# Kernel tuning notes

Measured on AMD Instinct MI355X. Metric: run time of the kernel, lower is better.

## Reference

```python
import jax, jax.numpy as jnp
import numpy as np

# Production-scale dims: ViT patch attention on a 32x32 patch grid
B, L, F = 16, 1024, 512      # batch, seq (=NX*NY patches), model dim
H, D = 8, 64                 # heads, head_dim (F = H*D)
NX, NY = 32, 32              # patch grid; Toeplitz table size 4*NX*NY = 4096


def setup_inputs() -> dict:
    key = jax.random.key(0)
    ks = jax.random.split(key, 12)
    w = lambda k, shp: jax.random.normal(k, shp, jnp.float32) * 0.02
    return {
        "inputs_q": jax.random.normal(ks[0], (B, L, F), jnp.float32),
        "inputs_kv": jax.random.normal(ks[1], (B, L, F), jnp.float32),
        "Wq": w(ks[2], (F, H * D)), "bq": jnp.zeros((H * D,), jnp.float32),
        "Wk": w(ks[3], (F, H * D)), "bk": jnp.zeros((H * D,), jnp.float32),
        "Wv": w(ks[4], (F, H * D)), "bv": jnp.zeros((H * D,), jnp.float32),
        "Wo": w(ks[5], (H * D, F)), "bo": jnp.zeros((F,), jnp.float32),
        "toeplitz": w(ks[6], (H, 4 * NX * NY)),
    }


def _rel_index():
    # 2D relative-position (Toeplitz) index: patch p -> (x, y) on NX x NY grid.
    coords = jnp.arange(L)
    xi, yi = coords // NY, coords % NY
    dx = xi[:, None] - xi[None, :] + NX          # in [1, 2*NX-1]
    dy = yi[:, None] - yi[None, :] + NY          # in [1, 2*NY-1]
    return dx * (2 * NY) + dy                    # [L, L] indices into 4*NX*NY table


def reference(inputs_q, inputs_kv, Wq, bq, Wk, bk, Wv, bv, Wo, bo, toeplitz):
    q = (inputs_q @ Wq + bq).reshape(B, L, H, D)
    k = (inputs_kv @ Wk + bk).reshape(B, L, H, D)
    v = (inputs_kv @ Wv + bv).reshape(B, L, H, D)
    bias = toeplitz[:, _rel_index()]             # [H, L, L] Toeplitz relative bias
    scale = 1.0 / jnp.sqrt(jnp.float32(D))
    scores = jnp.einsum("bqhd,bkhd->bhqk", q, k) * scale + bias  # [B,H,L,L]
    attn = jax.nn.softmax(scores, axis=-1)
    x = jnp.einsum("bhqk,bkhd->bqhd", attn, v).reshape(B, L, H * D)
    out = x @ Wo + bo
    return out.reshape(B, L, H, D)               # matches torch forward's final reshape
```

## Files before the change

### kernel.cpp

```cpp
#include <hip/hip_runtime.h>
#include <hip/hip_bf16.h>

#define B_  16
#define L_  1024
#define F_  512
#define H_  8
#define D_  64
#define M_  (B_ * L_)
#define HD_ 512

typedef __bf16 bf16x8 __attribute__((ext_vector_type(8)));
typedef __bf16 bf16x4 __attribute__((ext_vector_type(4)));
typedef short  s16x4  __attribute__((ext_vector_type(4)));
typedef float  f32x4  __attribute__((ext_vector_type(4)));

__device__ __forceinline__ void gl_lds16(const void* g, void* l) {
  __builtin_amdgcn_global_load_lds(
      (const __attribute__((address_space(1))) unsigned int*)g,
      (__attribute__((address_space(3))) unsigned int*)l, 16, 0, 0);
}

__global__ __launch_bounds__(256) void wt_kernel(
    const float* __restrict__ Wq, const float* __restrict__ Wk,
    const float* __restrict__ Wv, const float* __restrict__ Wo,
    __bf16* __restrict__ Wt_all)
{
  const float* W = (blockIdx.z == 0) ? Wq : (blockIdx.z == 1) ? Wk
                 : (blockIdx.z == 2) ? Wv : Wo;
  __bf16* Wt = Wt_all + (size_t)blockIdx.z * (512 * 512);
  __shared__ float s[32][33];
  const int t = threadIdx.x;
  const int r = t >> 5, c = t & 31;
  const int k0 = blockIdx.x * 32, n0 = blockIdx.y * 32;
#pragma unroll
  for (int i = 0; i < 4; ++i)
    s[r + i * 8][c] = W[(size_t)(k0 + r + i * 8) * 512 + n0 + c];
  __syncthreads();
#pragma unroll
  for (int i = 0; i < 4; ++i)
    Wt[(size_t)(n0 + r + i * 8) * 512 + k0 + c] = (__bf16)s[c][r + i * 8];
}

__global__ __launch_bounds__(256) void cvt_kernel(
    const float* __restrict__ xq, const float* __restrict__ xkv,
    __bf16* __restrict__ oq, __bf16* __restrict__ okv)
{
  const float* src = blockIdx.y ? xkv : xq;
  __bf16* dst = blockIdx.y ? okv : oq;
  size_t i = ((size_t)blockIdx.x * 256 + threadIdx.x) * 8;
  float4 f0 = *(const float4*)(src + i);
  float4 f1 = *(const float4*)(src + i + 4);
  bf16x8 v;
  v[0] = (__bf16)f0.x; v[1] = (__bf16)f0.y; v[2] = (__bf16)f0.z; v[3] = (__bf16)f0.w;
  v[4] = (__bf16)f1.x; v[5] = (__bf16)f1.y; v[6] = (__bf16)f1.z; v[7] = (__bf16)f1.w;
  *(bf16x8*)(dst + i) = v;
}

__global__ __launch_bounds__(256, 4) void gemm_proj_kernel(
    const __bf16* __restrict__ Xq, const __bf16* __restrict__ Xkv,
    const __bf16* __restrict__ Wt_all,
    const float* __restrict__ bq, const float* __restrict__ bk_,
    const float* __restrict__ bv_,
    __bf16* __restrict__ qd, __bf16* __restrict__ kd, __bf16* __restrict__ vd)
{
  const int seg = blockIdx.y >> 2;
  const __bf16* X = (seg == 0) ? Xq : Xkv;
  const __bf16* Wt = Wt_all + (size_t)seg * 262144;
  const float* bias = (seg == 0) ? bq : (seg == 1) ? bk_ : bv_;
  __bf16* dst = (seg == 0) ? qd : (seg == 1) ? kd : vd;
  const int mode = seg;

  __shared__ __align__(16) __bf16 As[2][4][128][8];
  __shared__ __align__(16) __bf16 Bs[2][4][128][8];
  const int t = threadIdx.x;
  const int m0 = blockIdx.x * 128, n0 = (blockIdx.y & 3) * 128;
  const int lane = t & 63, w = t >> 6;
  const int ml = lane & 15, quad = lane >> 4;
  const int wm = w & 1, wn = w >> 1;

  f32x4 acc[4][4];
#pragma unroll
  for (int i = 0; i < 4; ++i)
#pragma unroll
    for (int j = 0; j < 4; ++j) acc[i][j] = (f32x4){0.f, 0.f, 0.f, 0.f};

  const int slot0 = w * 64 + lane;
  const int slot1 = (w + 4) * 64 + lane;
  const int ko0 = slot0 >> 7, row0_ = slot0 & 127;
  const int ko1 = slot1 >> 7, row1_ = slot1 & 127;

#define STAGE_PROJ(buf, kk)                                                     \
  do {                                                                          \
    gl_lds16(&X[(size_t)(m0 + row0_) * 512 + (kk) + ko0 * 8],                   \
             &As[buf][ko0][row0_][0]);                                          \
    gl_lds16(&Wt[(size_t)(n0 + row0_) * 512 + (kk) + ko0 * 8],                  \
             &Bs[buf][ko0][row0_][0]);                                          \
    gl_lds16(&X[(size_t)(m0 + row1_) * 512 + (kk) + ko1 * 8],                   \
             &As[buf][ko1][row1_][0]);                                          \
    gl_lds16(&Wt[(size_t)(n0 + row1_) * 512 + (kk) + ko1 * 8],                  \
             &Bs[buf][ko1][row1_][0]);                                          \
  } while (0)

#define COMPUTE_TILE(buf)                                                       \
  do {                                                                          \
    bf16x8 a[4], b[4];                                                          \
    _Pragma("unroll") for (int mt = 0; mt < 4; ++mt)                            \
        a[mt] = *(const bf16x8*)&As[buf][quad][wm * 64 + mt * 16 + ml][0];      \
    _Pragma("unroll") for (int nt = 0; nt < 4; ++nt)                            \
        b[nt] = *(const bf16x8*)&Bs[buf][quad][wn * 64 + nt * 16 + ml][0];      \
    _Pragma("unroll") for (int mt = 0; mt < 4; ++mt)                            \
        _Pragma("unroll") for (int nt = 0; nt < 4; ++nt)                        \
            acc[mt][nt] = __builtin_amdgcn_mfma_f32_16x16x32_bf16(              \
                a[mt], b[nt], acc[mt][nt], 0, 0, 0);                            \
  } while (0)

  STAGE_PROJ(0, 0);
#pragma unroll
  for (int tt = 0; tt < 15; ++tt) {
    const int cur = tt & 1;
    STAGE_PROJ(cur ^ 1, (tt + 1) * 32);
    asm volatile("s_waitcnt vmcnt(4)" ::: "memory");
    asm volatile("s_barrier" ::: "memory");
    COMPUTE_TILE(cur);
    asm volatile("s_barrier" ::: "memory");
  }
  asm volatile("s_waitcnt vmcnt(0)" ::: "memory");
  asm volatile("s_barrier" ::: "memory");
  COMPUTE_TILE(1);

#pragma unroll
  for (int nt = 0; nt < 4; ++nt) {
    int col = n0 + wn * 64 + nt * 16 + ml;
    float bv = bias[col];
    int h = col >> 6, d = col & 63;
#pragma unroll
    for (int mt = 0; mt < 4; ++mt) {
      int row0 = m0 + wm * 64 + mt * 16 + quad * 4;
      int bz = row0 >> 10;
      int l0 = row0 & 1023;
      if (mode == 2) {
        bf16x4 pk;
#pragma unroll
        for (int r = 0; r < 4; ++r) pk[r] = (__bf16)(acc[mt][nt][r] + bv);
        size_t idx = ((size_t)(bz * H_ + h) * D_ + d) * L_ + l0;
        *(bf16x4*)&dst[idx] = pk;
      } else {
        size_t base = ((size_t)(bz * H_ + h) * L_ + l0) * D_ + d;
#pragma unroll
        for (int r = 0; r < 4; ++r)
          dst[base + (size_t)r * D_] = (__bf16)(acc[mt][nt][r] + bv);
      }
    }
  }
#undef STAGE_PROJ
#undef COMPUTE_TILE
}

__global__ __launch_bounds__(256, 2) void attn_kernel(
    const __bf16* __restrict__ qg,
    const __bf16* __restrict__ kg,
    const __bf16* __restrict__ vg,
    const float* __restrict__ toep_g,
    __bf16* __restrict__ xg)
{
  __shared__ float toep[4096];
  __shared__ __align__(16) __bf16 Ks[2][64][64];
  __shared__ __align__(16) __bf16 Vs[2][64][64];

  const int t = threadIdx.x;
  const int n = blockIdx.x;
  const int bh = ((n >> 5) << 3) | (n & 7);
  const int q0 = ((n >> 3) & 3) * 256;
  const int h = bh & 7;
  const int lane = t & 63, w = t >> 6;
  const int ml = lane & 15, quad = lane >> 4;
  const int lo3 = lane >> 3;
  const int kop = lane & 7;

  const size_t qkbase = (size_t)bh * (L_ * D_);
  const size_t vbase  = (size_t)bh * (D_ * L_);

  {
    const float4* src = (const float4*)(toep_g + (size_t)h * 4096);
    float4* dl = (float4*)toep;
    for (int i = t; i < 1024; i += 256) dl[i] = src[i];
  }

#pragma unroll
  for (int i = 0; i < 2; ++i) {
    int row = (w * 2 + i) * 8 + lo3;
    int ko = kop ^ lo3;
    gl_lds16(&kg[qkbase + (size_t)row * D_ + ko * 8], &Ks[0][row][kop * 8]);
    gl_lds16(&vg[vbase + (size_t)row * L_ + ko * 8], &Vs[0][row][kop * 8]);
  }

  bf16x8 qf[4][2];
#pragma unroll
  for (int qn = 0; qn < 4; ++qn) {
    const __bf16* qp =
        qg + qkbase + (size_t)(q0 + w * 64 + qn * 16 + ml) * D_ + quad * 8;
    qf[qn][0] = *(const bf16x8*)qp;
    qf[qn][1] = *(const bf16x8*)(qp + 32);
  }

  float lpart[4] = {0.f, 0.f, 0.f, 0.f};
  f32x4 o[4][4];
#pragma unroll
  for (int qn = 0; qn < 4; ++qn)
#pragma unroll
    for (int dt = 0; dt < 4; ++dt) o[qn][dt] = (f32x4){0.f, 0.f, 0.f, 0.f};

  __syncthreads();

  int cur = 0;
  for (int k0 = 0; k0 < L_; k0 += 64) {
    if (k0 + 64 < L_) {
      int nb = cur ^ 1;
#pragma unroll
      for (int i = 0; i < 2; ++i) {
        int row = (w * 2 + i) * 8 + lo3;
        int ko = kop ^ lo3;
        gl_lds16(&kg[qkbase + (size_t)(k0 + 64 + row) * D_ + ko * 8],
                 &Ks[nb][row][kop * 8]);
        gl_lds16(&vg[vbase + (size_t)row * L_ + k0 + 64 + ko * 8],
                 &Vs[nb][row][kop * 8]);
      }
    }

#pragma unroll
    for (int nt = 0; nt < 4; ++nt) {
      bf16x8 kf0 = *(const bf16x8*)&Ks[cur][nt * 16 + ml][(quad ^ (ml & 7)) * 8];
      bf16x8 kf1 =
          *(const bf16x8*)&Ks[cur][nt * 16 + ml][((4 + quad) ^ (ml & 7)) * 8];
      int kx = (k0 >> 5) + (nt >> 1);

      s16x4 pfrag[4];
#pragma unroll
      for (int qn = 0; qn < 4; ++qn) {
        f32x4 z = (f32x4){0.f, 0.f, 0.f, 0.f};
        z = __builtin_amdgcn_mfma_f32_16x16x32_bf16(kf0, qf[qn][0], z, 0, 0, 0);
        z = __builtin_amdgcn_mfma_f32_16x16x32_bf16(kf1, qf[qn][1], z, 0, 0, 0);

        int qb = w * 64 + qn * 16;
        int base = (((q0 + qb) >> 5) - kx + 32) * 64 +
                   ((qb & 31) + ml - ((nt & 1) * 16 + quad * 4) + 32);
        float p[4];
#pragma unroll
        for (int r = 0; r < 4; ++r)
          p[r] = __expf(fmaf(z[r], 0.125f, toep[base - r]));
        lpart[qn] += (p[0] + p[1]) + (p[2] + p[3]);
        bf16x4 pk;
#pragma unroll
        for (int r = 0; r < 4; ++r) pk[r] = (__bf16)p[r];
        pfrag[qn] = __builtin_bit_cast(s16x4, pk);
      }

#pragma unroll
      for (int dt = 0; dt < 4; ++dt) {
        int row = dt * 16 + ml;
        int gc = nt * 2 + (quad >> 1);
        bf16x4 vfr = *(const bf16x4*)
            &Vs[cur][row][((gc ^ (row & 7)) * 8) + (quad & 1) * 4];
        s16x4 vfs = __builtin_bit_cast(s16x4, vfr);
#pragma unroll
        for (int qn = 0; qn < 4; ++qn)
          o[qn][dt] = __builtin_amdgcn_mfma_f32_16x16x16bf16_1k(
              pfrag[qn], vfs, o[qn][dt], 0, 0, 0);
      }
    }

    __syncthreads();
    cur ^= 1;
  }

#pragma unroll
  for (int qn = 0; qn < 4; ++qn) {
    lpart[qn] += __shfl_xor(lpart[qn], 16);
    lpart[qn] += __shfl_xor(lpart[qn], 32);
  }
  float linv[4][4];
#pragma unroll
  for (int qn = 0; qn < 4; ++qn)
#pragma unroll
    for (int r = 0; r < 4; ++r)
      linv[qn][r] = 1.0f / __shfl(lpart[qn], quad * 16 + quad * 4 + r);

#pragma unroll
  for (int qn = 0; qn < 4; ++qn)
#pragma unroll
    for (int dt = 0; dt < 4; ++dt)
#pragma unroll
      for (int r = 0; r < 4; ++r) {
        int row = q0 + w * 64 + qn * 16 + quad * 4 + r;
        xg[((size_t)(bh >> 3) * L_ + row) * 512 + h * 64 + dt * 16 + ml] =
            (__bf16)(o[qn][dt][r] * linv[qn][r]);
      }
}

__global__ __launch_bounds__(256, 4) void gemm_out_kernel(
    const __bf16* __restrict__ Xb,
    const __bf16* __restrict__ Wt,
    const float* __restrict__ bo,
    float* __restrict__ out)
{
  __shared__ __align__(16) __bf16 As[2][4][128][8];
  __shared__ __align__(16) __bf16 Bs[2][4][128][8];
  const int t = threadIdx.x;
  const int m0 = blockIdx.x * 128, n0 = blockIdx.y * 128;
  const int lane = t & 63, w = t >> 6;
  const int ml = lane & 15, quad = lane >> 4;
  const int wm = w & 1, wn = w >> 1;

  f32x4 acc[4][4];
#pragma unroll
  for (int i = 0; i < 4; ++i)
#pragma unroll
    for (int j = 0; j < 4; ++j) acc[i][j] = (f32x4){0.f, 0.f, 0.f, 0.f};

  const int slot0 = w * 64 + lane;
  const int slot1 = (w + 4) * 64 + lane;
  const int ko0 = slot0 >> 7, row0_ = slot0 & 127;
  const int ko1 = slot1 >> 7, row1_ = slot1 & 127;

#define STAGE_OUT(buf, kk)                                                      \
  do {                                                                          \
    gl_lds16(&Xb[(size_t)(m0 + row0_) * 512 + (kk) + ko0 * 8],                  \
             &As[buf][ko0][row0_][0]);                                          \
    gl_lds16(&Wt[(size_t)(n0 + row0_) * 512 + (kk) + ko0 * 8],                  \
             &Bs[buf][ko0][row0_][0]);                                          \
    gl_lds16(&Xb[(size_t)(m0 + row1_) * 512 + (kk) + ko1 * 8],                  \
             &As[buf][ko1][row1_][0]);                                          \
    gl_lds16(&Wt[(size_t)(n0 + row1_) * 512 + (kk) + ko1 * 8],                  \
             &Bs[buf][ko1][row1_][0]);                                          \
  } while (0)

#define COMPUTE_TILE_O(buf)                                                     \
  do {                                                                          \
    bf16x8 a[4], b[4];                                                          \
    _Pragma("unroll") for (int mt = 0; mt < 4; ++mt)                            \
        a[mt] = *(const bf16x8*)&As[buf][quad][wm * 64 + mt * 16 + ml][0];      \
    _Pragma("unroll") for (int nt = 0; nt < 4; ++nt)                            \
        b[nt] = *(const bf16x8*)&Bs[buf][quad][wn * 64 + nt * 16 + ml][0];      \
    _Pragma("unroll") for (int mt = 0; mt < 4; ++mt)                            \
        _Pragma("unroll") for (int nt = 0; nt < 4; ++nt)                        \
            acc[mt][nt] = __builtin_amdgcn_mfma_f32_16x16x32_bf16(              \
                a[mt], b[nt], acc[mt][nt], 0, 0, 0);                            \
  } while (0)

  STAGE_OUT(0, 0);
#pragma unroll
  for (int tt = 0; tt < 15; ++tt) {
    const int cur = tt & 1;
    STAGE_OUT(cur ^ 1, (tt + 1) * 32);
    asm volatile("s_waitcnt vmcnt(4)" ::: "memory");
    asm volatile("s_barrier" ::: "memory");
    COMPUTE_TILE_O(cur);
    asm volatile("s_barrier" ::: "memory");
  }
  asm volatile("s_waitcnt vmcnt(0)" ::: "memory");
  asm volatile("s_barrier" ::: "memory");
  COMPUTE_TILE_O(1);

#pragma unroll
  for (int nt = 0; nt < 4; ++nt) {
    int col = n0 + wn * 64 + nt * 16 + ml;
    float bv = bo[col];
#pragma unroll
    for (int mt = 0; mt < 4; ++mt) {
      int row0 = m0 + wm * 64 + mt * 16 + quad * 4;
#pragma unroll
      for (int r = 0; r < 4; ++r)
        out[(size_t)(row0 + r) * 512 + col] = acc[mt][nt][r] + bv;
    }
  }
#undef STAGE_OUT
#undef COMPUTE_TILE_O
}

extern "C" void kernel_launch(void* const* d_in, const int* in_sizes, int n_in,
                              void* d_out, int out_size, void* d_ws, size_t ws_size,
                              hipStream_t stream) {
  const float* inputs_q  = (const float*)d_in[0];
  const float* inputs_kv = (const float*)d_in[1];
  const float* Wq = (const float*)d_in[2];
  const float* bq = (const float*)d_in[3];
  const float* Wk = (const float*)d_in[4];
  const float* bk = (const float*)d_in[5];
  const float* Wv = (const float*)d_in[6];
  const float* bv = (const float*)d_in[7];
  const float* Wo = (const float*)d_in[8];
  const float* bo = (const float*)d_in[9];
  const float* toep = (const float*)d_in[10];
  float* out = (float*)d_out;

  char* ws = (char*)d_ws;
  __bf16* qb  = (__bf16*)(ws);
  __bf16* kb  = (__bf16*)(ws + 16777216);
  __bf16* vb  = (__bf16*)(ws + 33554432);
  __bf16* xb  = (__bf16*)(ws + 50331648);
  __bf16* Wt  = (__bf16*)(ws + 67108864);
  __bf16* xqb = (__bf16*)(ws + 69206016);
  __bf16* xkvb = xb;

  wt_kernel<<<dim3(16, 16, 4), 256, 0, stream>>>(Wq, Wk, Wv, Wo, Wt);
  cvt_kernel<<<dim3(4096, 2), 256, 0, stream>>>(inputs_q, inputs_kv, xqb, xkvb);
  gemm_proj_kernel<<<dim3(128, 12), 256, 0, stream>>>(
      xqb, xkvb, Wt, bq, bk, bv, qb, kb, vb);
  attn_kernel<<<dim3(512), 256, 0, stream>>>(qb, kb, vb, toep, xb);
  gemm_out_kernel<<<dim3(128, 4), 256, 0, stream>>>(xb, Wt + 3 * 262144, bo, out);
}
```

Baseline: 270.8 us.

## Fuse fp32-to-bf16 input conversion into projection GEMM and cache Toeplitz bias in registers

Removes the separate conversion kernel: the projection GEMM now loads fp32 activations into registers, converts them to bf16 and writes them to LDS, while weights are still staged asynchronously. The projection launch is split into two launches of six column-block groups each. In attention, the nine Toeplitz bias values each lane needs per key tile are preloaded into registers rather than indexed from LDS inside the inner loop. This saves one round trip through the bf16 copy of the inputs, but the projection GEMM now reads twice as many A bytes per tile (fp32) and uses register-staged loads instead of direct global-to-LDS copies. It also adds one more kernel launch and more register pressure.

Result: faster. 262.4 us (-3.1%).

```diff
diff --git a/kernel.cpp b/kernel.cpp
--- a/kernel.cpp
+++ b/kernel.cpp
@@ -41,30 +41,17 @@
     Wt[(size_t)(n0 + r + i * 8) * 512 + k0 + c] = (__bf16)s[c][r + i * 8];
 }
 
-__global__ __launch_bounds__(256) void cvt_kernel(
-    const float* __restrict__ xq, const float* __restrict__ xkv,
-    __bf16* __restrict__ oq, __bf16* __restrict__ okv)
-{
-  const float* src = blockIdx.y ? xkv : xq;
-  __bf16* dst = blockIdx.y ? okv : oq;
-  size_t i = ((size_t)blockIdx.x * 256 + threadIdx.x) * 8;
-  float4 f0 = *(const float4*)(src + i);
-  float4 f1 = *(const float4*)(src + i + 4);
-  bf16x8 v;
-  v[0] = (__bf16)f0.x; v[1] = (__bf16)f0.y; v[2] = (__bf16)f0.z; v[3] = (__bf16)f0.w;
-  v[4] = (__bf16)f1.x; v[5] = (__bf16)f1.y; v[6] = (__bf16)f1.z; v[7] = (__bf16)f1.w;
-  *(bf16x8*)(dst + i) = v;
-}
-
-__global__ __launch_bounds__(256, 4) void gemm_proj_kernel(
-    const __bf16* __restrict__ Xq, const __bf16* __restrict__ Xkv,
+__global__ __launch_bounds__(256) void gemm_proj_kernel(
+    const float* __restrict__ Xq, const float* __restrict__ Xkv,
     const __bf16* __restrict__ Wt_all,
     const float* __restrict__ bq, const float* __restrict__ bk_,
     const float* __restrict__ bv_,
-    __bf16* __restrict__ qd, __bf16* __restrict__ kd, __bf16* __restrict__ vd)
+    __bf16* __restrict__ qd, __bf16* __restrict__ kd, __bf16* __restrict__ vd,
+    int ybase)
 {
-  const int seg = blockIdx.y >> 2;
-  const __bf16* X = (seg == 0) ? Xq : Xkv;
+  const int by = blockIdx.y + ybase;
+  const int seg = by >> 2;
+  const float* X = (seg == 0) ? Xq : Xkv;
   const __bf16* Wt = Wt_all + (size_t)seg * 262144;
   const float* bias = (seg == 0) ? bq : (seg == 1) ? bk_ : bv_;
   __bf16* dst = (seg == 0) ? qd : (seg == 1) ? kd : vd;
@@ -73,7 +60,7 @@
   __shared__ __align__(16) __bf16 As[2][4][128][8];
   __shared__ __align__(16) __bf16 Bs[2][4][128][8];
   const int t = threadIdx.x;
-  const int m0 = blockIdx.x * 128, n0 = (blockIdx.y & 3) * 128;
+  const int m0 = blockIdx.x * 128, n0 = (by & 3) * 128;
   const int lane = t & 63, w = t >> 6;
   const int ml = lane & 15, quad = lane >> 4;
   const int wm = w & 1, wn = w >> 1;
@@ -84,21 +71,41 @@
 #pragma unroll
     for (int j = 0; j < 4; ++j) acc[i][j] = (f32x4){0.f, 0.f, 0.f, 0.f};
 
-  const int slot0 = w * 64 + lane;
-  const int slot1 = (w + 4) * 64 + lane;
-  const int ko0 = slot0 >> 7, row0_ = slot0 & 127;
-  const int ko1 = slot1 >> 7, row1_ = slot1 & 127;
-
-#define STAGE_PROJ(buf, kk)                                                     \
-  do {                                                                          \
-    gl_lds16(&X[(size_t)(m0 + row0_) * 512 + (kk) + ko0 * 8],                   \
-             &As[buf][ko0][row0_][0]);                                          \
-    gl_lds16(&Wt[(size_t)(n0 + row0_) * 512 + (kk) + ko0 * 8],                  \
-             &Bs[buf][ko0][row0_][0]);                                          \
-    gl_lds16(&X[(size_t)(m0 + row1_) * 512 + (kk) + ko1 * 8],                   \
-             &As[buf][ko1][row1_][0]);                                          \
-    gl_lds16(&Wt[(size_t)(n0 + row1_) * 512 + (kk) + ko1 * 8],                  \
-             &Bs[buf][ko1][row1_][0]);                                          \
+  const int ako0 = t & 3,          arow0 = t >> 2;
+  const int ako1 = (t + 256) & 3,  arow1 = (t + 256) >> 2;
+  const int bs0 = w * 64 + lane,   bs1 = (w + 4) * 64 + lane;
+  const int bko0 = bs0 >> 7, brow0 = bs0 & 127;
+  const int bko1 = bs1 >> 7, brow1 = bs1 & 127;
+
+  float4 fa0, fa1, fa2, fa3;
+
+#define ALOAD(kk)                                                               \
+  do {                                                                          \
+    const float* p0 = X + (size_t)(m0 + arow0) * 512 + (kk) + ako0 * 8;         \
+    const float* p1 = X + (size_t)(m0 + arow1) * 512 + (kk) + ako1 * 8;         \
+    fa0 = *(const float4*)p0; fa1 = *(const float4*)(p0 + 4);                   \
+    fa2 = *(const float4*)p1; fa3 = *(const float4*)(p1 + 4);                   \
+  } while (0)
+
+#define AWRITE(buf)                                                             \
+  do {                                                                          \
+    bf16x8 v0, v1;                                                              \
+    v0[0] = (__bf16)fa0.x; v0[1] = (__bf16)fa0.y; v0[2] = (__bf16)fa0.z;        \
+    v0[3] = (__bf16)fa0.w; v0[4] = (__bf16)fa1.x; v0[5] = (__bf16)fa1.y;        \
+    v0[6] = (__bf16)fa1.z; v0[7] = (__bf16)fa1.w;                               \
+    v1[0] = (__bf16)fa2.x; v1[1] = (__bf16)fa2.y; v1[2] = (__bf16)fa2.z;        \
+    v1[3] = (__bf16)fa2.w; v1[4] = (__bf16)fa3.x; v1[5] = (__bf16)fa3.y;        \
+    v1[6] = (__bf16)fa3.z; v1[7] = (__bf16)fa3.w;                               \
+    *(bf16x8*)&As[buf][ako0][arow0][0] = v0;                                    \
+    *(bf16x8*)&As[buf][ako1][arow1][0] = v1;                                    \
+  } while (0)
+
+#define BSTAGE(buf, kk)                                                         \
+  do {                                                                          \
+    gl_lds16(&Wt[(size_t)(n0 + brow0) * 512 + (kk) + bko0 * 8],                 \
+             &Bs[buf][bko0][brow0][0]);                                         \
+    gl_lds16(&Wt[(size_t)(n0 + brow1) * 512 + (kk) + bko1 * 8],                 \
+             &Bs[buf][bko1][brow1][0]);                                         \
   } while (0)
 
 #define COMPUTE_TILE(buf)                                                       \
@@ -114,18 +121,20 @@
                 a[mt], b[nt], acc[mt][nt], 0, 0, 0);                            \
   } while (0)
 
-  STAGE_PROJ(0, 0);
+  BSTAGE(0, 0);
+  ALOAD(0);
+  AWRITE(0);
+  __syncthreads();
+
 #pragma unroll
   for (int tt = 0; tt < 15; ++tt) {
-    const int cur = tt & 1;
-    STAGE_PROJ(cur ^ 1, (tt + 1) * 32);
-    asm volatile("s_waitcnt vmcnt(4)" ::: "memory");
-    asm volatile("s_barrier" ::: "memory");
+    const int cur = tt & 1, nxt = cur ^ 1;
+    ALOAD((tt + 1) * 32);
+    BSTAGE(nxt, (tt + 1) * 32);
     COMPUTE_TILE(cur);
-    asm volatile("s_barrier" ::: "memory");
-  }
-  asm volatile("s_waitcnt vmcnt(0)" ::: "memory");
-  asm volatile("s_barrier" ::: "memory");
+    AWRITE(nxt);
+    __syncthreads();
+  }
   COMPUTE_TILE(1);
 
 #pragma unroll
@@ -152,7 +161,9 @@
       }
     }
   }
-#undef STAGE_PROJ
+#undef ALOAD
+#undef AWRITE
+#undef BSTAGE
 #undef COMPUTE_TILE
 }
 
@@ -227,12 +238,23 @@
       }
     }
 
+    const int cb0 = (((q0 + w * 64) >> 5) - (k0 >> 5) + 31) * 64 +
+                    (ml - quad * 4 + 16);
+    float tc[3][3][4];
+#pragma unroll
+    for (int a = 0; a < 3; ++a)
+#pragma unroll
+      for (int b = 0; b < 3; ++b) {
+        const int cb = cb0 + a * 64 + b * 16;
+#pragma unroll
+        for (int r = 0; r < 4; ++r) tc[a][b][r] = toep[cb - r];
+      }
+
 #pragma unroll
     for (int nt = 0; nt < 4; ++nt) {
       bf16x8 kf0 = *(const bf16x8*)&Ks[cur][nt * 16 + ml][(quad ^ (ml & 7)) * 8];
       bf16x8 kf1 =
           *(const bf16x8*)&Ks[cur][nt * 16 + ml][((4 + quad) ^ (ml & 7)) * 8];
-      int kx = (k0 >> 5) + (nt >> 1);
 
       s16x4 pfrag[4];
 #pragma unroll
@@ -241,13 +263,12 @@
         z = __builtin_amdgcn_mfma_f32_16x16x32_bf16(kf0, qf[qn][0], z, 0, 0, 0);
         z = __builtin_amdgcn_mfma_f32_16x16x32_bf16(kf1, qf[qn][1], z, 0, 0, 0);
 
-        int qb = w * 64 + qn * 16;
-        int base = (((q0 + qb) >> 5) - kx + 32) * 64 +
-                   ((qb & 31) + ml - ((nt & 1) * 16 + quad * 4) + 32);
         float p[4];
 #pragma unroll
         for (int r = 0; r < 4; ++r)
-          p[r] = __expf(fmaf(z[r], 0.125f, toep[base - r]));
+          p[r] = __expf(fmaf(z[r], 0.125f,
+                             tc[(qn >> 1) - (nt >> 1) + 1]
+                               [(qn & 1) - (nt & 1) + 1][r]));
         lpart[qn] += (p[0] + p[1]) + (p[2] + p[3]);
         bf16x4 pk;
 #pragma unroll
@@ -399,13 +420,12 @@
   __bf16* vb  = (__bf16*)(ws + 33554432);
   __bf16* xb  = (__bf16*)(ws + 50331648);
   __bf16* Wt  = (__bf16*)(ws + 67108864);
-  __bf16* xqb = (__bf16*)(ws + 69206016);
-  __bf16* xkvb = xb;
 
   wt_kernel<<<dim3(16, 16, 4), 256, 0, stream>>>(Wq, Wk, Wv, Wo, Wt);
-  cvt_kernel<<<dim3(4096, 2), 256, 0, stream>>>(inputs_q, inputs_kv, xqb, xkvb);
-  gemm_proj_kernel<<<dim3(128, 12), 256, 0, stream>>>(
-      xqb, xkvb, Wt, bq, bk, bv, qb, kb, vb);
+  gemm_proj_kernel<<<dim3(128, 6), 256, 0, stream>>>(
+      inputs_q, inputs_kv, Wt, bq, bk, bv, qb, kb, vb, 0);
+  gemm_proj_kernel<<<dim3(128, 6), 256, 0, stream>>>(
+      inputs_q, inputs_kv, Wt, bq, bk, bv, qb, kb, vb, 6);
   attn_kernel<<<dim3(512), 256, 0, stream>>>(qb, kb, vb, toep, xb);
   gemm_out_kernel<<<dim3(128, 4), 256, 0, stream>>>(xb, Wt + 3 * 262144, bo, out);
 }
```
